# Kernel tuning notes

Hardware: AMD Instinct MI355X
Metric: run time of the kernel (lower is better)

The kernel has to match this reference:

```python
import jax, jax.numpy as jnp
import numpy as np

B, T, E = 2, 2048, 2048
H, H_KV, D = 16, 8, 128
THETA = 10000.0


def setup_inputs() -> dict:
    key = jax.random.key(0)
    ks = jax.random.split(key, 5)
    s = lambda n: (1.0 / np.sqrt(n))
    x = jax.random.normal(ks[0], (B, T, E), dtype=jnp.float32)
    wq = jax.random.normal(ks[1], (E, H * D), dtype=jnp.float32) * s(E)
    wk = jax.random.normal(ks[2], (E, H_KV * D), dtype=jnp.float32) * s(E)
    wv = jax.random.normal(ks[3], (E, H_KV * D), dtype=jnp.float32) * s(E)
    wo = jax.random.normal(ks[4], (H * D, E), dtype=jnp.float32) * s(H * D)
    # causal mask, broadcast over batch and heads
    mask = jnp.tril(jnp.ones((T, T), dtype=jnp.int32))[None, None, :, :]
    return {"x": x, "mask": mask, "wq": wq, "wk": wk, "wv": wv, "wo": wo}


def _rope(q, k):
    # q,k: [B,H,T,D]; deinterleave even/odd, rotate, concat halves (as in source)
    Tq, Dh = q.shape[2], q.shape[3] // 2
    inv = 1.0 / (THETA ** (jnp.arange(Dh, dtype=jnp.float32) / Dh))
    ang = jnp.arange(Tq, dtype=jnp.float32)[:, None] * inv[None, :]  # [T,Dh]
    c, s = jnp.cos(ang), jnp.sin(ang)  # broadcast over [B,H]
    q1, q2 = q[..., ::2], q[..., 1::2]
    k1, k2 = k[..., ::2], k[..., 1::2]
    q_rot = jnp.concatenate([q1 * c - q2 * s, q2 * c + q1 * s], axis=-1)
    k_rot = jnp.concatenate([k1 * c - k2 * s, k2 * c + k1 * s], axis=-1)
    return q_rot, k_rot


def reference(x, mask, wq, wk, wv, wo):
    Bx, Tx, _ = x.shape
    scale = D ** -0.5
    q = (x @ wq).reshape(Bx, Tx, H, D).transpose(0, 2, 1, 3)      # [B,H,T,D]
    k = (x @ wk).reshape(Bx, Tx, H_KV, D).transpose(0, 2, 1, 3)   # [B,Hkv,T,D]
    v = (x @ wv).reshape(Bx, Tx, H_KV, D).transpose(0, 2, 1, 3)
    # torch .repeat tiles along head axis: [kv0..kv7, kv0..kv7]
    k = jnp.tile(k, (1, H // H_KV, 1, 1))
    v = jnp.tile(v, (1, H // H_KV, 1, 1))
    q, k = _rope(q, k)
    attn = jnp.einsum('bhtd,bhsd->bhts', q, k) * scale
    attn = jnp.where(mask == 0, -jnp.inf, attn)
    w = jax.nn.softmax(attn, axis=-1)
    w = jnp.where(jnp.isnan(w), 0.0, w)
    out = jnp.einsum('bhts,bhsd->bhtd', w, v)
    out = out.transpose(0, 2, 1, 3).reshape(Bx, Tx, H * D)
    return out @ wo
```

## Files before the change

kernel.cpp:

```cpp
#include <hip/hip_runtime.h>
#include <hip/hip_bf16.h>
#include <cstdint>

typedef short bf16x8 __attribute__((ext_vector_type(8)));
typedef float f32x4 __attribute__((ext_vector_type(4)));
typedef unsigned short u16;
typedef unsigned int u32;

#define TT 2048

__device__ __forceinline__ u16 f2bf(float f) {
    __hip_bfloat16 h = __float2bfloat16(f);
    return __builtin_bit_cast(u16, h);
}
__device__ __forceinline__ float bf2f(u16 u) {
    return __builtin_bit_cast(float, (u32)u << 16);
}
__device__ __forceinline__ f32x4 mfma16(bf16x8 a, bf16x8 b, f32x4 c) {
    return __builtin_amdgcn_mfma_f32_16x16x32_bf16(a, b, c, 0, 0, 0);
}
__device__ __forceinline__ bf16x8 ldg8(const u16* p) {
    return __builtin_bit_cast(bf16x8, *reinterpret_cast<const uint4*>(p));
}
__device__ __forceinline__ bf16x8 lds8(const u16* p) {
    return *reinterpret_cast<const bf16x8*>(p);
}
__device__ __forceinline__ void gll16(const u16* g, u16* l) {
    __builtin_amdgcn_global_load_lds(
        (const __attribute__((address_space(1))) void*)g,
        (__attribute__((address_space(3))) void*)l, 16, 0, 0);
}

#define ASMBAR asm volatile("s_barrier" ::: "memory")
#define WAIT_VM8 asm volatile("s_waitcnt vmcnt(8)" ::: "memory")
#define WAIT_VM0 asm volatile("s_waitcnt vmcnt(0)" ::: "memory")
#define WAIT_LGKM0 asm volatile("s_waitcnt lgkmcnt(0)" ::: "memory")

__global__ __launch_bounds__(256) void prologue(const float* __restrict__ x,
                                                const float* __restrict__ wq,
                                                const float* __restrict__ wk,
                                                const float* __restrict__ wv,
                                                const float* __restrict__ wo,
                                                u16* __restrict__ xb,
                                                u16* __restrict__ wqkvT,
                                                u16* __restrict__ woT) {
    const int z = blockIdx.z;
    const int tid = threadIdx.x;
    if (z == 4) {
        int bix = blockIdx.y * 32 + blockIdx.x;
#pragma unroll
        for (int k = 0; k < 4; k++) {
            int idx = (bix * 1024 + k * 256 + tid) * 8;
            float4 a = *reinterpret_cast<const float4*>(&x[idx]);
            float4 b = *reinterpret_cast<const float4*>(&x[idx + 4]);
            u16 o[8] = {f2bf(a.x), f2bf(a.y), f2bf(a.z), f2bf(a.w),
                        f2bf(b.x), f2bf(b.y), f2bf(b.z), f2bf(b.w)};
            *reinterpret_cast<uint4*>(&xb[idx]) = *reinterpret_cast<const uint4*>(o);
        }
        return;
    }
    const float* src;
    u16* dst;
    int C, rope;
    const int R = 2048;
    if (z == 0) { src = wq; dst = wqkvT;               C = 2048; rope = 1; }
    else if (z == 1) { src = wk; dst = wqkvT + 2048 * 2048; C = 1024; rope = 1; }
    else if (z == 2) { src = wv; dst = wqkvT + 3072 * 2048; C = 1024; rope = 0; }
    else { src = wo; dst = woT;                        C = 2048; rope = 0; }
    const int cb = blockIdx.x, rb = blockIdx.y;
    if (cb * 64 >= C) return;

    __shared__ float tl[64][65];
#pragma unroll
    for (int i = 0; i < 16; i++) {
        int li = i * 256 + tid;
        int tr = li >> 6, tc = li & 63;
        tl[tr][tc] = src[(size_t)(rb * 64 + tr) * C + cb * 64 + tc];
    }
    __syncthreads();
#pragma unroll
    for (int i = 0; i < 16; i++) {
        int li = i * 256 + tid;
        int dr = li >> 6, dc = li & 63;
        int c = cb * 64 + dr;
        int j;
        if (rope) {
            int head = c >> 7, cl = c & 127, ii = cl >> 1, odd = cl & 1;
            j = head * 128 + ((ii & 15) | (odd << 4) | ((ii >> 4) << 5));
        } else {
            j = c;
        }
        dst[(size_t)j * R + rb * 64 + dc] = f2bf(tl[dc][dr]);
    }
}

template <int MODE>
__global__ __launch_bounds__(512, 2) void gemm256(const u16* __restrict__ A,
                                                  const u16* __restrict__ BT,
                                                  void* __restrict__ P0, void* __restrict__ P1,
                                                  void* __restrict__ P2, int M, int N, int K) {
    __shared__ __align__(16) u16 smA[2][256 * 64];
    __shared__ __align__(16) u16 smB[2][256 * 64];
    const int tid = threadIdx.x;
    const int w = tid >> 6, lane = tid & 63, quad = lane >> 4, l15 = lane & 15;
    const int wr = w >> 2, wc = w & 3;
    const int bm = blockIdx.y, bn = blockIdx.x;

    f32x4 acc[8][4];
    const f32x4 zf = {0.f, 0.f, 0.f, 0.f};
#pragma unroll
    for (int i = 0; i < 8; i++)
#pragma unroll
        for (int j = 0; j < 4; j++) acc[i][j] = zf;

    const u16* aSrc[4];
    const u16* bSrc[4];
#pragma unroll
    for (int i = 0; i < 4; i++) {
        int o = i * 512 + tid;
        int r = o >> 3, p = o & 7;
        int cc = p ^ (r & 7);
        aSrc[i] = A + (size_t)(bm * 256 + r) * K + cc * 8;
        bSrc[i] = BT + (size_t)(bn * 256 + r) * K + cc * 8;
    }
    auto stage = [&](int buf) {
#pragma unroll
        for (int i = 0; i < 4; i++) {
            gll16(aSrc[i], &smA[buf][(i * 512 + w * 64) * 8]);
            aSrc[i] += 64;
        }
#pragma unroll
        for (int i = 0; i < 4; i++) {
            gll16(bSrc[i], &smB[buf][(i * 512 + w * 64) * 8]);
            bSrc[i] += 64;
        }
    };

    stage(0);
    stage(1);
    WAIT_VM8;
    ASMBAR;

    const int nkt = K >> 6;
    for (int kt = 0; kt < nkt; ++kt) {
        const int cur = kt & 1;
        bf16x8 a[4][2], b01[2][2], b23[2][2];
#pragma unroll
        for (int mi = 0; mi < 4; mi++)
#pragma unroll
            for (int ks = 0; ks < 2; ks++) {
                int row = wr * 128 + mi * 16 + l15, cd = ks * 4 + quad;
                a[mi][ks] = lds8(&smA[cur][row * 64 + ((cd ^ (row & 7)) * 8)]);
            }
#pragma unroll
        for (int ni = 0; ni < 2; ni++)
#pragma unroll
            for (int ks = 0; ks < 2; ks++) {
                int row = wc * 64 + ni * 16 + l15, cd = ks * 4 + quad;
                b01[ni][ks] = lds8(&smB[cur][row * 64 + ((cd ^ (row & 7)) * 8)]);
            }
        ASMBAR;
        __builtin_amdgcn_s_setprio(1);
#pragma unroll
        for (int mi = 0; mi < 4; mi++)
#pragma unroll
            for (int ni = 0; ni < 2; ni++)
#pragma unroll
                for (int ks = 0; ks < 2; ks++)
                    acc[mi][ni] = mfma16(a[mi][ks], b01[ni][ks], acc[mi][ni]);
        __builtin_amdgcn_s_setprio(0);
        ASMBAR;
#pragma unroll
        for (int ni = 0; ni < 2; ni++)
#pragma unroll
            for (int ks = 0; ks < 2; ks++) {
                int row = wc * 64 + (ni + 2) * 16 + l15, cd = ks * 4 + quad;
                b23[ni][ks] = lds8(&smB[cur][row * 64 + ((cd ^ (row & 7)) * 8)]);
            }
        ASMBAR;
        __builtin_amdgcn_s_setprio(1);
#pragma unroll
        for (int mi = 0; mi < 4; mi++)
#pragma unroll
            for (int ni = 0; ni < 2; ni++)
#pragma unroll
                for (int ks = 0; ks < 2; ks++)
                    acc[mi][ni + 2] = mfma16(a[mi][ks], b23[ni][ks], acc[mi][ni + 2]);
        __builtin_amdgcn_s_setprio(0);
        ASMBAR;
#pragma unroll
        for (int mi = 0; mi < 4; mi++)
#pragma unroll
            for (int ks = 0; ks < 2; ks++) {
                int row = wr * 128 + (mi + 4) * 16 + l15, cd = ks * 4 + quad;
                a[mi][ks] = lds8(&smA[cur][row * 64 + ((cd ^ (row & 7)) * 8)]);
            }
        ASMBAR;
        __builtin_amdgcn_s_setprio(1);
#pragma unroll
        for (int mi = 0; mi < 4; mi++)
#pragma unroll
            for (int ni = 0; ni < 2; ni++)
#pragma unroll
                for (int ks = 0; ks < 2; ks++)
                    acc[mi + 4][ni + 2] = mfma16(a[mi][ks], b23[ni][ks], acc[mi + 4][ni + 2]);
        __builtin_amdgcn_s_setprio(0);
        WAIT_LGKM0;
        ASMBAR;
        if (kt + 2 < nkt) stage(cur);
        ASMBAR;
        __builtin_amdgcn_s_setprio(1);
#pragma unroll
        for (int mi = 0; mi < 4; mi++)
#pragma unroll
            for (int ni = 0; ni < 2; ni++)
#pragma unroll
                for (int ks = 0; ks < 2; ks++)
                    acc[mi + 4][ni] = mfma16(a[mi][ks], b01[ni][ks], acc[mi + 4][ni]);
        __builtin_amdgcn_s_setprio(0);
        if (kt + 2 < nkt) { WAIT_VM8; }
        else if (kt + 1 < nkt) { WAIT_VM0; }
        ASMBAR;
    }

    if (MODE == 1) {
#pragma unroll
        for (int mi = 0; mi < 8; mi++)
#pragma unroll
            for (int ni = 0; ni < 4; ni++)
#pragma unroll
                for (int r = 0; r < 4; r++) {
                    int m = bm * 256 + wr * 128 + mi * 16 + quad * 4 + r;
                    int n = bn * 256 + wc * 64 + ni * 16 + l15;
                    ((float*)P0)[(size_t)m * N + n] = acc[mi][ni][r];
                }
    } else if (bn < 12) {
#pragma unroll
        for (int mi = 0; mi < 8; mi++)
#pragma unroll
            for (int g = 0; g < 2; g++) {
                int i = ((wc & 1) * 2 + g) * 16 + l15;
                float inv = __expf(-0.14391156644f * (float)i);
#pragma unroll
                for (int r = 0; r < 4; r++) {
                    int m = bm * 256 + wr * 128 + mi * 16 + quad * 4 + r;
                    int b = m >> 11, t = m & 2047;
                    float ang = (float)t * inv;
                    float sn, cs;
                    __sincosf(ang, &sn, &cs);
                    float x1 = acc[mi][2 * g][r], x2 = acc[mi][2 * g + 1][r];
                    u16 o1 = f2bf(x1 * cs - x2 * sn);
                    u16 o2 = f2bf(x2 * cs + x1 * sn);
                    if (bn < 8) {
                        int h = bn * 2 + (wc >> 1);
                        u16* pq = (u16*)P0 + ((size_t)(b * 16 + h) * 2048 + t) * 128;
                        pq[i] = o1;
                        pq[i + 64] = o2;
                    } else {
                        int hk = (bn - 8) * 2 + (wc >> 1);
                        u16* pk = (u16*)P1 + ((size_t)(b * 8 + hk) * 2048 + t) * 128;
                        pk[i] = o1;
                        pk[i + 64] = o2;
                    }
                }
            }
    } else {
#pragma unroll
        for (int mi = 0; mi < 8; mi++)
#pragma unroll
            for (int ni = 0; ni < 4; ni++)
#pragma unroll
                for (int r = 0; r < 4; r++) {
                    int m = bm * 256 + wr * 128 + mi * 16 + quad * 4 + r;
                    int b = m >> 11, t = m & 2047;
                    int d = (wc & 1) * 64 + ni * 16 + l15;
                    int h = (bn - 12) * 2 + (wc >> 1);
                    ((u16*)P2)[((size_t)(b * 8 + h) * 128 + d) * 2048 + t] =
                        f2bf(acc[mi][ni][r]);
                }
    }
}

__global__ __launch_bounds__(256) void flash_attn(const u16* __restrict__ qg,
                                                  const u16* __restrict__ kg,
                                                  const u16* __restrict__ vg,
                                                  u16* __restrict__ og) {
    __shared__ __align__(16) u16 Ksm[2][64 * 128];
    __shared__ __align__(16) u16 Vsm[2][128 * 64];
    __shared__ __align__(16) u16 Pt[4 * 32 * 64];
    const int tid = threadIdx.x, w = tid >> 6, lane = tid & 63, quad = lane >> 4,
              l15 = lane & 15;
    const int bkv = blockIdx.x;
    const int qblk = 31 - (int)blockIdx.y;
    const int b = bkv >> 3, kvh = bkv & 7;
    const float scale = 0.08838834764831845f;

    const u16* kb = kg + (size_t)(b * 8 + kvh) * 2048 * 128;
    const u16* vb = vg + (size_t)(b * 8 + kvh) * 128 * 2048;

    bf16x8 aq[2][4];
#pragma unroll
    for (int hh = 0; hh < 2; hh++) {
        const int h = kvh + hh * 8;
        const u16* qp =
            qg + ((size_t)(b * 16 + h) * 2048 + qblk * 64 + w * 16 + l15) * 128 + quad * 8;
#pragma unroll
        for (int kk = 0; kk < 4; kk++) aq[hh][kk] = ldg8(qp + kk * 32);
    }

    f32x4 oacc[2][8];
    f32x4 lacc[2];
    const f32x4 zf = {0.f, 0.f, 0.f, 0.f};
#pragma unroll
    for (int hh = 0; hh < 2; hh++) {
        lacc[hh] = zf;
#pragma unroll
        for (int j = 0; j < 8; j++) oacc[hh][j] = zf;
    }
    bf16x8 ones;
#pragma unroll
    for (int i = 0; i < 8; i++) ones[i] = (short)0x3F80;

    auto stage = [&](int st, int buf) {
#pragma unroll
        for (int i = 0; i < 4; i++) {
            int o = i * 256 + w * 64 + lane;
            int s = o >> 4, p = o & 15;
            int cc = (p & 8) | ((p ^ s) & 7);
            gll16(kb + (size_t)(st * 64 + s) * 128 + cc * 8, &Ksm[buf][(i * 256 + w * 64) * 8]);
            int d = o >> 3, p2 = o & 7;
            int cc2 = (p2 ^ d) & 7;
            gll16(vb + (size_t)d * 2048 + st * 64 + cc2 * 8, &Vsm[buf][(i * 256 + w * 64) * 8]);
        }
    };

    stage(0, 0);
    for (int st = 0; st <= qblk; ++st) {
        const int cur = st & 1;
        __syncthreads();
        if (st < qblk) stage(st + 1, cur ^ 1);

        f32x4 s0[4], s1[4];
#pragma unroll
        for (int j = 0; j < 4; j++) {
            s0[j] = zf;
            s1[j] = zf;
#pragma unroll
            for (int kk = 0; kk < 4; kk++) {
                int srow = j * 16 + l15;
                int cd = kk * 4 + quad;
                int p = (cd & 8) | ((cd ^ srow) & 7);
                bf16x8 bk = lds8(&Ksm[cur][srow * 128 + p * 8]);
                s0[j] = mfma16(aq[0][kk], bk, s0[j]);
                s1[j] = mfma16(aq[1][kk], bk, s1[j]);
            }
        }
        const bool diag = (st == qblk);
#pragma unroll
        for (int j = 0; j < 4; j++)
#pragma unroll
            for (int r = 0; r < 4; r++) {
                bool masked = diag && (j * 16 + l15) > (w * 16 + quad * 4 + r);
                float p0 = masked ? 0.f : __expf(s0[j][r] * scale);
                float p1 = masked ? 0.f : __expf(s1[j][r] * scale);
                int prow = w * 32 + quad * 4 + r;
                int cc = (j * 2 + (l15 >> 3));
                int off = (l15 & 7);
                Pt[prow * 64 + ((cc ^ (prow & 7)) * 8) + off] = f2bf(p0);
                int prow1 = prow + 16;
                Pt[prow1 * 64 + ((cc ^ (prow1 & 7)) * 8) + off] = f2bf(p1);
            }
#pragma unroll
        for (int kk = 0; kk < 2; kk++) {
            int row0 = w * 32 + l15, row1 = row0 + 16;
            int cd2 = kk * 4 + quad;
            bf16x8 ap0 = lds8(&Pt[row0 * 64 + ((cd2 ^ (row0 & 7)) * 8)]);
            bf16x8 ap1 = lds8(&Pt[row1 * 64 + ((cd2 ^ (row1 & 7)) * 8)]);
#pragma unroll
            for (int jf = 0; jf < 8; jf++) {
                int drow = jf * 16 + l15;
                int p2 = (cd2 ^ drow) & 7;
                bf16x8 bv = lds8(&Vsm[cur][drow * 64 + p2 * 8]);
                oacc[0][jf] = mfma16(ap0, bv, oacc[0][jf]);
                oacc[1][jf] = mfma16(ap1, bv, oacc[1][jf]);
            }
            lacc[0] = mfma16(ap0, ones, lacc[0]);
            lacc[1] = mfma16(ap1, ones, lacc[1]);
        }
    }
#pragma unroll
    for (int hh = 0; hh < 2; hh++) {
        const int h = kvh + hh * 8;
#pragma unroll
        for (int jf = 0; jf < 8; jf++)
#pragma unroll
            for (int r = 0; r < 4; r++) {
                int t = qblk * 64 + w * 16 + quad * 4 + r;
                int d = jf * 16 + l15;
                og[((size_t)(b * 2048 + t) * 16 + h) * 128 + d] =
                    f2bf(oacc[hh][jf][r] / lacc[hh][r]);
            }
    }
}

extern "C" void kernel_launch(void* const* d_in, const int* in_sizes, int n_in, void* d_out,
                              int out_size, void* d_ws, size_t ws_size, hipStream_t stream) {
    const float* x = (const float*)d_in[0];
    const float* wq = (const float*)d_in[2];
    const float* wk = (const float*)d_in[3];
    const float* wv = (const float*)d_in[4];
    const float* wo = (const float*)d_in[5];
    float* out = (float*)d_out;

    char* ws = (char*)d_ws;
    u16* xb = (u16*)(ws);
    u16* wqkvT = (u16*)(ws + 16777216);
    u16* woT = (u16*)(ws + 33554432);
    u16* qbuf = (u16*)(ws + 41943040);
    u16* kbuf = (u16*)(ws + 58720256);
    u16* vtb = (u16*)(ws + 67108864);
    u16* obuf = xb;

    prologue<<<dim3(32, 32, 5), 256, 0, stream>>>(x, wq, wk, wv, wo, xb, wqkvT, woT);

    gemm256<0><<<dim3(16, 16), 512, 0, stream>>>(xb, wqkvT, qbuf, kbuf, vtb, 4096, 4096, 2048);

    flash_attn<<<dim3(16, 32), 256, 0, stream>>>(qbuf, kbuf, vtb, obuf);

    gemm256<1><<<dim3(8, 16), 512, 0, stream>>>(obuf, woT, out, nullptr, nullptr, 4096, 2048,
                                                2048);
}
```

Before: 341.5 us.

## Split GEMM loads into half-tile stages, add 128-tile output GEMM, vectorize transpose stores

The QKV projection GEMM now loads the A and B tiles as separate 128-row halves. The loop body is unrolled over two k-tiles, so each half's next load can be issued as soon as that half's LDS reads finish, giving finer-grained overlap of global-to-LDS copies with MFMA work. The output projection moves to a new 256-thread kernel with 128x128 tiles, launching 512 blocks instead of 128 to fill more compute units. The prologue weight transpose now writes 8 bf16 values per 16-byte store instead of scalar stores. The finer waitcnt/barrier choreography risks hazards or extra stalls if the counts are wrong.

```diff
diff --git a/kernel.cpp b/kernel.cpp
--- a/kernel.cpp
+++ b/kernel.cpp
@@ -33,7 +33,9 @@
 
 #define ASMBAR asm volatile("s_barrier" ::: "memory")
 #define WAIT_VM8 asm volatile("s_waitcnt vmcnt(8)" ::: "memory")
+#define WAIT_VM4 asm volatile("s_waitcnt vmcnt(4)" ::: "memory")
 #define WAIT_VM0 asm volatile("s_waitcnt vmcnt(0)" ::: "memory")
+#define WAIT_LGKM8 asm volatile("s_waitcnt lgkmcnt(8)" ::: "memory")
 #define WAIT_LGKM0 asm volatile("s_waitcnt lgkmcnt(0)" ::: "memory")
 
 __global__ __launch_bounds__(256) void prologue(const float* __restrict__ x,
@@ -79,9 +81,9 @@
     }
     __syncthreads();
 #pragma unroll
-    for (int i = 0; i < 16; i++) {
-        int li = i * 256 + tid;
-        int dr = li >> 6, dc = li & 63;
+    for (int i = 0; i < 2; i++) {
+        int task = i * 256 + tid;
+        int dr = task >> 3, dc0 = (task & 7) * 8;
         int c = cb * 64 + dr;
         int j;
         if (rope) {
@@ -90,15 +92,18 @@
         } else {
             j = c;
         }
-        dst[(size_t)j * R + rb * 64 + dc] = f2bf(tl[dc][dr]);
-    }
-}
-
-template <int MODE>
-__global__ __launch_bounds__(512, 2) void gemm256(const u16* __restrict__ A,
-                                                  const u16* __restrict__ BT,
-                                                  void* __restrict__ P0, void* __restrict__ P1,
-                                                  void* __restrict__ P2, int M, int N, int K) {
+        u16 o[8];
+#pragma unroll
+        for (int k2 = 0; k2 < 8; k2++) o[k2] = f2bf(tl[dc0 + k2][dr]);
+        *reinterpret_cast<uint4*>(&dst[(size_t)j * R + rb * 64 + dc0]) =
+            *reinterpret_cast<const uint4*>(o);
+    }
+}
+
+__global__ __launch_bounds__(512, 2) void gemm8p(const u16* __restrict__ A,
+                                                 const u16* __restrict__ BT,
+                                                 u16* __restrict__ Pq, u16* __restrict__ Pk,
+                                                 u16* __restrict__ Pv, int M, int N, int K) {
     __shared__ __align__(16) u16 smA[2][256 * 64];
     __shared__ __align__(16) u16 smB[2][256 * 64];
     const int tid = threadIdx.x;
@@ -113,128 +118,189 @@
 #pragma unroll
         for (int j = 0; j < 4; j++) acc[i][j] = zf;
 
-    const u16* aSrc[4];
-    const u16* bSrc[4];
-#pragma unroll
-    for (int i = 0; i < 4; i++) {
+    const u16* aPtr[2];
+    const u16* bPtr[2];
+#pragma unroll
+    for (int i = 0; i < 2; i++) {
         int o = i * 512 + tid;
         int r = o >> 3, p = o & 7;
         int cc = p ^ (r & 7);
-        aSrc[i] = A + (size_t)(bm * 256 + r) * K + cc * 8;
-        bSrc[i] = BT + (size_t)(bn * 256 + r) * K + cc * 8;
-    }
-    auto stage = [&](int buf) {
-#pragma unroll
-        for (int i = 0; i < 4; i++) {
-            gll16(aSrc[i], &smA[buf][(i * 512 + w * 64) * 8]);
-            aSrc[i] += 64;
-        }
-#pragma unroll
-        for (int i = 0; i < 4; i++) {
-            gll16(bSrc[i], &smB[buf][(i * 512 + w * 64) * 8]);
-            bSrc[i] += 64;
-        }
+        aPtr[i] = A + (size_t)(bm * 256 + r) * K + cc * 8;
+        bPtr[i] = BT + (size_t)(bn * 256 + r) * K + cc * 8;
+    }
+    auto stageA = [&](int h, int buf, int kt) {
+#pragma unroll
+        for (int i = 0; i < 2; i++)
+            gll16(aPtr[i] + (size_t)h * 128 * K + kt * 64,
+                  &smA[buf][h * 8192 + (i * 512 + w * 64) * 8]);
     };
-
-    stage(0);
-    stage(1);
-    WAIT_VM8;
+    auto stageB = [&](int h, int buf, int kt) {
+#pragma unroll
+        for (int i = 0; i < 2; i++)
+            gll16(bPtr[i] + (size_t)h * 128 * K + kt * 64,
+                  &smB[buf][h * 8192 + (i * 512 + w * 64) * 8]);
+    };
+    auto rdA = [&](int c, int mrow, int ks) {
+        int row = wr * 128 + mrow * 16 + l15, cd = ks * 4 + quad;
+        return lds8(&smA[c][row * 64 + ((cd ^ (row & 7)) * 8)]);
+    };
+    auto rdB = [&](int c, int ni, int ks) {
+        int row = wc * 64 + ni * 16 + l15, cd = ks * 4 + quad;
+        return lds8(&smB[c][row * 64 + ((cd ^ (row & 7)) * 8)]);
+    };
+
+    stageA(0, 0, 0); stageA(1, 0, 0); stageB(0, 0, 0); stageB(1, 0, 0);
+    stageB(0, 1, 1); stageB(1, 1, 1);
+    WAIT_VM4;
     ASMBAR;
 
-    const int nkt = K >> 6;
-    for (int kt = 0; kt < nkt; ++kt) {
-        const int cur = kt & 1;
-        bf16x8 a[4][2], b01[2][2], b23[2][2];
-#pragma unroll
-        for (int mi = 0; mi < 4; mi++)
-#pragma unroll
-            for (int ks = 0; ks < 2; ks++) {
-                int row = wr * 128 + mi * 16 + l15, cd = ks * 4 + quad;
-                a[mi][ks] = lds8(&smA[cur][row * 64 + ((cd ^ (row & 7)) * 8)]);
-            }
+    const int nkt = K >> 6, niter = nkt >> 1;
+    for (int it = 0; it < niter; ++it) {
+        const int t2 = 2 * it + 2, t3 = 2 * it + 3;
+        const bool more = (it + 1 < niter);
+        bf16x8 aL[4][2], aH[4][2], b01[2][2], b23[2][2];
+
+#pragma unroll
+        for (int mi = 0; mi < 4; mi++)
+#pragma unroll
+            for (int ks = 0; ks < 2; ks++) aL[mi][ks] = rdA(0, mi, ks);
 #pragma unroll
         for (int ni = 0; ni < 2; ni++)
 #pragma unroll
-            for (int ks = 0; ks < 2; ks++) {
-                int row = wc * 64 + ni * 16 + l15, cd = ks * 4 + quad;
-                b01[ni][ks] = lds8(&smB[cur][row * 64 + ((cd ^ (row & 7)) * 8)]);
-            }
-        ASMBAR;
-        __builtin_amdgcn_s_setprio(1);
-#pragma unroll
-        for (int mi = 0; mi < 4; mi++)
-#pragma unroll
-            for (int ni = 0; ni < 2; ni++)
-#pragma unroll
-                for (int ks = 0; ks < 2; ks++)
-                    acc[mi][ni] = mfma16(a[mi][ks], b01[ni][ks], acc[mi][ni]);
+            for (int ks = 0; ks < 2; ks++) b01[ni][ks] = rdB(0, ni, ks);
+        stageA(0, 1, 2 * it + 1);
+        WAIT_LGKM8;
+        ASMBAR;
+        WAIT_LGKM0;
+        __builtin_amdgcn_s_setprio(1);
+#pragma unroll
+        for (int mi = 0; mi < 4; mi++)
+#pragma unroll
+            for (int ni = 0; ni < 2; ni++)
+#pragma unroll
+                for (int ks = 0; ks < 2; ks++)
+                    acc[mi][ni] = mfma16(aL[mi][ks], b01[ni][ks], acc[mi][ni]);
         __builtin_amdgcn_s_setprio(0);
         ASMBAR;
 #pragma unroll
         for (int ni = 0; ni < 2; ni++)
 #pragma unroll
-            for (int ks = 0; ks < 2; ks++) {
-                int row = wc * 64 + (ni + 2) * 16 + l15, cd = ks * 4 + quad;
-                b23[ni][ks] = lds8(&smB[cur][row * 64 + ((cd ^ (row & 7)) * 8)]);
-            }
-        ASMBAR;
-        __builtin_amdgcn_s_setprio(1);
-#pragma unroll
-        for (int mi = 0; mi < 4; mi++)
-#pragma unroll
-            for (int ni = 0; ni < 2; ni++)
-#pragma unroll
-                for (int ks = 0; ks < 2; ks++)
-                    acc[mi][ni + 2] = mfma16(a[mi][ks], b23[ni][ks], acc[mi][ni + 2]);
-        __builtin_amdgcn_s_setprio(0);
-        ASMBAR;
-#pragma unroll
-        for (int mi = 0; mi < 4; mi++)
-#pragma unroll
-            for (int ks = 0; ks < 2; ks++) {
-                int row = wr * 128 + (mi + 4) * 16 + l15, cd = ks * 4 + quad;
-                a[mi][ks] = lds8(&smA[cur][row * 64 + ((cd ^ (row & 7)) * 8)]);
-            }
-        ASMBAR;
-        __builtin_amdgcn_s_setprio(1);
-#pragma unroll
-        for (int mi = 0; mi < 4; mi++)
-#pragma unroll
-            for (int ni = 0; ni < 2; ni++)
-#pragma unroll
-                for (int ks = 0; ks < 2; ks++)
-                    acc[mi + 4][ni + 2] = mfma16(a[mi][ks], b23[ni][ks], acc[mi + 4][ni + 2]);
-        __builtin_amdgcn_s_setprio(0);
+            for (int ks = 0; ks < 2; ks++) b23[ni][ks] = rdB(0, ni + 2, ks);
+        stageA(1, 1, 2 * it + 1);
+        ASMBAR;
         WAIT_LGKM0;
-        ASMBAR;
-        if (kt + 2 < nkt) stage(cur);
-        ASMBAR;
-        __builtin_amdgcn_s_setprio(1);
-#pragma unroll
-        for (int mi = 0; mi < 4; mi++)
-#pragma unroll
-            for (int ni = 0; ni < 2; ni++)
-#pragma unroll
-                for (int ks = 0; ks < 2; ks++)
-                    acc[mi + 4][ni] = mfma16(a[mi][ks], b01[ni][ks], acc[mi + 4][ni]);
-        __builtin_amdgcn_s_setprio(0);
-        if (kt + 2 < nkt) { WAIT_VM8; }
-        else if (kt + 1 < nkt) { WAIT_VM0; }
-        ASMBAR;
-    }
-
-    if (MODE == 1) {
-#pragma unroll
-        for (int mi = 0; mi < 8; mi++)
-#pragma unroll
-            for (int ni = 0; ni < 4; ni++)
-#pragma unroll
-                for (int r = 0; r < 4; r++) {
-                    int m = bm * 256 + wr * 128 + mi * 16 + quad * 4 + r;
-                    int n = bn * 256 + wc * 64 + ni * 16 + l15;
-                    ((float*)P0)[(size_t)m * N + n] = acc[mi][ni][r];
-                }
-    } else if (bn < 12) {
+        __builtin_amdgcn_s_setprio(1);
+#pragma unroll
+        for (int mi = 0; mi < 4; mi++)
+#pragma unroll
+            for (int ni = 0; ni < 2; ni++)
+#pragma unroll
+                for (int ks = 0; ks < 2; ks++)
+                    acc[mi][ni + 2] = mfma16(aL[mi][ks], b23[ni][ks], acc[mi][ni + 2]);
+        __builtin_amdgcn_s_setprio(0);
+        ASMBAR;
+#pragma unroll
+        for (int mi = 0; mi < 4; mi++)
+#pragma unroll
+            for (int ks = 0; ks < 2; ks++) aH[mi][ks] = rdA(0, mi + 4, ks);
+        if (more) stageB(0, 0, t2);
+        ASMBAR;
+        WAIT_LGKM0;
+        __builtin_amdgcn_s_setprio(1);
+#pragma unroll
+        for (int mi = 0; mi < 4; mi++)
+#pragma unroll
+            for (int ni = 0; ni < 2; ni++)
+#pragma unroll
+                for (int ks = 0; ks < 2; ks++)
+                    acc[mi + 4][ni + 2] = mfma16(aH[mi][ks], b23[ni][ks], acc[mi + 4][ni + 2]);
+        __builtin_amdgcn_s_setprio(0);
+        ASMBAR;
+        if (more) stageB(1, 0, t2);
+        ASMBAR;
+        __builtin_amdgcn_s_setprio(1);
+#pragma unroll
+        for (int mi = 0; mi < 4; mi++)
+#pragma unroll
+            for (int ni = 0; ni < 2; ni++)
+#pragma unroll
+                for (int ks = 0; ks < 2; ks++)
+                    acc[mi + 4][ni] = mfma16(aH[mi][ks], b01[ni][ks], acc[mi + 4][ni]);
+        __builtin_amdgcn_s_setprio(0);
+        if (more) { WAIT_VM4; } else { WAIT_VM0; }
+        ASMBAR;
+#pragma unroll
+        for (int mi = 0; mi < 4; mi++)
+#pragma unroll
+            for (int ks = 0; ks < 2; ks++) aL[mi][ks] = rdA(1, mi, ks);
+#pragma unroll
+        for (int ni = 0; ni < 2; ni++)
+#pragma unroll
+            for (int ks = 0; ks < 2; ks++) b01[ni][ks] = rdB(1, ni, ks);
+        if (more) stageA(0, 0, t2);
+        WAIT_LGKM8;
+        ASMBAR;
+        WAIT_LGKM0;
+        __builtin_amdgcn_s_setprio(1);
+#pragma unroll
+        for (int mi = 0; mi < 4; mi++)
+#pragma unroll
+            for (int ni = 0; ni < 2; ni++)
+#pragma unroll
+                for (int ks = 0; ks < 2; ks++)
+                    acc[mi][ni] = mfma16(aL[mi][ks], b01[ni][ks], acc[mi][ni]);
+        __builtin_amdgcn_s_setprio(0);
+        ASMBAR;
+#pragma unroll
+        for (int ni = 0; ni < 2; ni++)
+#pragma unroll
+            for (int ks = 0; ks < 2; ks++) b23[ni][ks] = rdB(1, ni + 2, ks);
+        if (more) stageA(1, 0, t2);
+        ASMBAR;
+        WAIT_LGKM0;
+        __builtin_amdgcn_s_setprio(1);
+#pragma unroll
+        for (int mi = 0; mi < 4; mi++)
+#pragma unroll
+            for (int ni = 0; ni < 2; ni++)
+#pragma unroll
+                for (int ks = 0; ks < 2; ks++)
+                    acc[mi][ni + 2] = mfma16(aL[mi][ks], b23[ni][ks], acc[mi][ni + 2]);
+        __builtin_amdgcn_s_setprio(0);
+        ASMBAR;
+#pragma unroll
+        for (int mi = 0; mi < 4; mi++)
+#pragma unroll
+            for (int ks = 0; ks < 2; ks++) aH[mi][ks] = rdA(1, mi + 4, ks);
+        if (more) stageB(0, 1, t3);
+        ASMBAR;
+        WAIT_LGKM0;
+        __builtin_amdgcn_s_setprio(1);
+#pragma unroll
+        for (int mi = 0; mi < 4; mi++)
+#pragma unroll
+            for (int ni = 0; ni < 2; ni++)
+#pragma unroll
+                for (int ks = 0; ks < 2; ks++)
+                    acc[mi + 4][ni + 2] = mfma16(aH[mi][ks], b23[ni][ks], acc[mi + 4][ni + 2]);
+        __builtin_amdgcn_s_setprio(0);
+        ASMBAR;
+        if (more) stageB(1, 1, t3);
+        ASMBAR;
+        __builtin_amdgcn_s_setprio(1);
+#pragma unroll
+        for (int mi = 0; mi < 4; mi++)
+#pragma unroll
+            for (int ni = 0; ni < 2; ni++)
+#pragma unroll
+                for (int ks = 0; ks < 2; ks++)
+                    acc[mi + 4][ni] = mfma16(aH[mi][ks], b01[ni][ks], acc[mi + 4][ni]);
+        __builtin_amdgcn_s_setprio(0);
+        WAIT_VM4;
+        ASMBAR;
+    }
+
+    if (bn < 12) {
 #pragma unroll
         for (int mi = 0; mi < 8; mi++)
 #pragma unroll
@@ -253,12 +319,12 @@
                     u16 o2 = f2bf(x2 * cs + x1 * sn);
                     if (bn < 8) {
                         int h = bn * 2 + (wc >> 1);
-                        u16* pq = (u16*)P0 + ((size_t)(b * 16 + h) * 2048 + t) * 128;
+                        u16* pq = Pq + ((size_t)(b * 16 + h) * 2048 + t) * 128;
                         pq[i] = o1;
                         pq[i + 64] = o2;
                     } else {
                         int hk = (bn - 8) * 2 + (wc >> 1);
-                        u16* pk = (u16*)P1 + ((size_t)(b * 8 + hk) * 2048 + t) * 128;
+                        u16* pk = Pk + ((size_t)(b * 8 + hk) * 2048 + t) * 128;
                         pk[i] = o1;
                         pk[i + 64] = o2;
                     }
@@ -275,10 +341,85 @@
                     int b = m >> 11, t = m & 2047;
                     int d = (wc & 1) * 64 + ni * 16 + l15;
                     int h = (bn - 12) * 2 + (wc >> 1);
-                    ((u16*)P2)[((size_t)(b * 8 + h) * 128 + d) * 2048 + t] =
-                        f2bf(acc[mi][ni][r]);
+                    Pv[((size_t)(b * 8 + h) * 128 + d) * 2048 + t] = f2bf(acc[mi][ni][r]);
                 }
     }
+}
+
+__global__ __launch_bounds__(256) void gemm_o(const u16* __restrict__ A,
+                                              const u16* __restrict__ BT,
+                                              float* __restrict__ C, int M, int N, int K) {
+    __shared__ __align__(16) u16 smA[2][128 * 64];
+    __shared__ __align__(16) u16 smB[2][128 * 64];
+    const int tid = threadIdx.x;
+    const int w = tid >> 6, lane = tid & 63, quad = lane >> 4, l15 = lane & 15;
+    const int wr = w >> 1, wc = w & 1;
+    const int bm = blockIdx.y, bn = blockIdx.x;
+
+    f32x4 acc[4][4];
+    const f32x4 zf = {0.f, 0.f, 0.f, 0.f};
+#pragma unroll
+    for (int i = 0; i < 4; i++)
+#pragma unroll
+        for (int j = 0; j < 4; j++) acc[i][j] = zf;
+
+    const u16* aSrc[4];
+    const u16* bSrc[4];
+#pragma unroll
+    for (int i = 0; i < 4; i++) {
+        int o = i * 256 + tid;
+        int r = o >> 3, p = o & 7;
+        int cc = p ^ (r & 7);
+        aSrc[i] = A + (size_t)(bm * 128 + r) * K + cc * 8;
+        bSrc[i] = BT + (size_t)(bn * 128 + r) * K + cc * 8;
+    }
+    auto stage = [&](int buf) {
+#pragma unroll
+        for (int i = 0; i < 4; i++) {
+            gll16(aSrc[i], &smA[buf][(i * 256 + w * 64) * 8]);
+            gll16(bSrc[i], &smB[buf][(i * 256 + w * 64) * 8]);
+            aSrc[i] += 64;
+            bSrc[i] += 64;
+        }
+    };
+
+    stage(0);
+    const int nkt = K >> 6;
+    for (int kt = 0; kt < nkt; ++kt) {
+        const int cur = kt & 1;
+        __syncthreads();
+        if (kt + 1 < nkt) stage(cur ^ 1);
+#pragma unroll
+        for (int ks = 0; ks < 2; ++ks) {
+            const int cd = ks * 4 + quad;
+            bf16x8 af[4], bf[4];
+#pragma unroll
+            for (int mi = 0; mi < 4; mi++) {
+                int row = wr * 64 + mi * 16 + l15;
+                af[mi] = lds8(&smA[cur][row * 64 + (cd ^ (row & 7)) * 8]);
+            }
+#pragma unroll
+            for (int ni = 0; ni < 4; ni++) {
+                int row = wc * 64 + ni * 16 + l15;
+                bf[ni] = lds8(&smB[cur][row * 64 + (cd ^ (row & 7)) * 8]);
+            }
+#pragma unroll
+            for (int mi = 0; mi < 4; mi++)
+#pragma unroll
+                for (int ni = 0; ni < 4; ni++) acc[mi][ni] = mfma16(af[mi], bf[ni], acc[mi][ni]);
+        }
+    }
+
+#pragma unroll
+    for (int mi = 0; mi < 4; mi++)
+#pragma unroll
+        for (int ni = 0; ni < 4; ni++)
+#pragma unroll
+            for (int r = 0; r < 4; r++) {
+                int m = bm * 128 + wr * 64 + mi * 16 + quad * 4 + r;
+                int n = bn * 128 + wc * 64 + ni * 16 + l15;
+                C[(size_t)m * N + n] = acc[mi][ni][r];
+            }
 }
 
 __global__ __launch_bounds__(256) void flash_attn(const u16* __restrict__ qg,
@@ -423,10 +564,9 @@
 
     prologue<<<dim3(32, 32, 5), 256, 0, stream>>>(x, wq, wk, wv, wo, xb, wqkvT, woT);
 
-    gemm256<0><<<dim3(16, 16), 512, 0, stream>>>(xb, wqkvT, qbuf, kbuf, vtb, 4096, 4096, 2048);
+    gemm8p<<<dim3(16, 16), 512, 0, stream>>>(xb, wqkvT, qbuf, kbuf, vtb, 4096, 4096, 2048);
 
     flash_attn<<<dim3(16, 32), 256, 0, stream>>>(qbuf, kbuf, vtb, obuf);
 
-    gemm256<1><<<dim3(8, 16), 512, 0, stream>>>(obuf, woT, out, nullptr, nullptr, 4096, 2048,
-                                                2048);
-}
+    gemm_o<<<dim3(16, 32), 256, 0, stream>>>(obuf, woT, out, 4096, 2048, 2048);
+}
```

New measurement: 308.5 us. 1.11x faster.
